# Kernel optimization log

Measured on AMD Instinct MI355X. Metric: run time of the kernel, lower is better.

Reference implementation:

```python
import jax, jax.numpy as jnp
import numpy as np

EPS = 1e-5  # BatchNorm1d default eps
N1, N2 = 4096, 4096


def _encoder(x, W1, b1, W2, b2, W3, b3, gamma, beta):
    # fc1: Linear(node_num,256)+ReLU; fc2: Linear(256,128)+ReLU; fc3: Linear(128,64)+BN(train-mode)+ReLU
    h = jax.nn.relu(x @ W1.T + b1)
    h = jax.nn.relu(h @ W2.T + b2)
    h = h @ W3.T + b3
    m = h.mean(axis=0)
    v = ((h - m) ** 2).mean(axis=0)  # biased variance, as BN training mode
    return jax.nn.relu((h - m) / jnp.sqrt(v + EPS) * gamma + beta)


def _self_attention(x, adj, alpha):
    # vectorized form of the per-node double loop:
    # tmp_i = (sum_{j: adj[i,j]==1} alpha[i,j] * x[j]) / degree_i + x[i]  if degree_i != 0 else 0
    mask = (adj == 1.0).astype(x.dtype)           # [N,N]
    deg = adj.sum(axis=1, keepdims=True)          # [N,1]
    agg = (mask * alpha) @ x                      # [N,64] masked SpMM
    return jnp.where(deg != 0, agg / deg + x, jnp.zeros((), x.dtype))


def setup_inputs() -> dict:
    key = jax.random.key(0)
    ks = jax.random.split(key, 20)
    d = {}
    d["x1"] = jax.random.normal(ks[0], (N1, N1), jnp.float32)
    d["x2"] = jax.random.normal(ks[1], (N2, N2), jnp.float32)
    d["adj1"] = jax.random.bernoulli(ks[2], 0.01, (N1, N1)).astype(jnp.float32)
    d["adj2"] = jax.random.bernoulli(ks[3], 0.01, (N2, N2)).astype(jnp.float32)
    def lin(k, fan_out, fan_in):
        bound = 1.0 / np.sqrt(fan_in)
        k1, k2 = jax.random.split(k)
        return (jax.random.uniform(k1, (fan_out, fan_in), jnp.float32, -bound, bound),
                jax.random.uniform(k2, (fan_out,), jnp.float32, -bound, bound))
    d["e1_W1"], d["e1_b1"] = lin(ks[4], 256, N1)
    d["e1_W2"], d["e1_b2"] = lin(ks[5], 128, 256)
    d["e1_W3"], d["e1_b3"] = lin(ks[6], 64, 128)
    d["e1_gamma"] = jnp.ones((64,), jnp.float32)
    d["e1_beta"] = jnp.zeros((64,), jnp.float32)
    d["e2_W1"], d["e2_b1"] = lin(ks[7], 256, N2)
    d["e2_W2"], d["e2_b2"] = lin(ks[8], 128, 256)
    d["e2_W3"], d["e2_b3"] = lin(ks[9], 64, 128)
    d["e2_gamma"] = jnp.ones((64,), jnp.float32)
    d["e2_beta"] = jnp.zeros((64,), jnp.float32)
    d["alpha1"] = jax.random.uniform(ks[10], (N1, N1), jnp.float32)
    d["alpha2"] = jax.random.uniform(ks[11], (N2, N2), jnp.float32)
    d["Wc"], d["bc"] = lin(ks[12], 2, (N1 + N2) * 64)
    return d


def reference(x1, x2, adj1, adj2,
              e1_W1, e1_b1, e1_W2, e1_b2, e1_W3, e1_b3, e1_gamma, e1_beta,
              e2_W1, e2_b1, e2_W2, e2_b2, e2_W3, e2_b3, e2_gamma, e2_beta,
              alpha1, alpha2, Wc, bc):
    h1 = _encoder(x1, e1_W1, e1_b1, e1_W2, e1_b2, e1_W3, e1_b3, e1_gamma, e1_beta)
    h2 = _encoder(x2, e2_W1, e2_b1, e2_W2, e2_b2, e2_W3, e2_b3, e2_gamma, e2_beta)
    h1 = _self_attention(h1, adj1, alpha1)
    h2 = _self_attention(h2, adj2, alpha2)
    feat = jnp.concatenate([h1, h2], axis=0).reshape(1, -1)  # [1,(N1+N2)*64]
    return feat @ Wc.T + bc  # [1,2] logits (softmax is defined but unused in forward)
```

## Files before the change

### kernel.cpp

```cpp
#include <hip/hip_runtime.h>
#include <cstddef>


#define NN 4096
#define HDIM 64
#define ENC_OUT (NN * HDIM)

typedef _Float16 half8 __attribute__((ext_vector_type(8)));
typedef _Float16 half4 __attribute__((ext_vector_type(4)));
typedef float v4f __attribute__((ext_vector_type(4)));

struct GemmP {
    const void*     A[2];
    const _Float16* B[2];
    const float*    bias[2];
    void*           C[2];
};

template<int NI, bool A_HALF, bool RELU, bool HALF_OUT>
__global__ __launch_bounds__(256) void gemm32_kernel(GemmP p, int K)
{
    constexpr int N = NI * 64;
    __shared__ _Float16 As[32][40];
    __shared__ _Float16 Bs[N][40];

    const int tid = threadIdx.x;
    const int wave = tid >> 6, lane = tid & 63;
    const int quad = lane >> 4, l16 = lane & 15;
    const int enc = blockIdx.z;
    const int m0 = blockIdx.y * 32;

    const _Float16* __restrict__ Bp = p.B[enc];

    const int ar = tid >> 3, ak = (tid & 7) * 4;
    const int br = tid >> 2, bk = (tid & 3) * 8;

    v4f acc[2][NI];
#pragma unroll
    for (int mi = 0; mi < 2; mi++)
#pragma unroll
        for (int ni = 0; ni < NI; ni++) acc[mi][ni] = (v4f){0.f, 0.f, 0.f, 0.f};

    for (int k0 = 0; k0 < K; k0 += 32) {
        __syncthreads();
        if (A_HALF) {
            const _Float16* ap = (const _Float16*)p.A[enc] + (size_t)(m0 + ar) * K + k0 + ak;
            *(half4*)&As[ar][ak] = *(const half4*)ap;
        } else {
            const float* ap = (const float*)p.A[enc] + (size_t)(m0 + ar) * K + k0 + ak;
            float4 a = *(const float4*)ap;
            half4 h;
            h[0] = (_Float16)a.x; h[1] = (_Float16)a.y;
            h[2] = (_Float16)a.z; h[3] = (_Float16)a.w;
            *(half4*)&As[ar][ak] = h;
        }
#pragma unroll
        for (int pass = 0; pass < NI; pass++) {
            const _Float16* bp = Bp + (size_t)(pass * 64 + br) * K + k0 + bk;
            *(half8*)&Bs[pass * 64 + br][bk] = *(const half8*)bp;
        }
        __syncthreads();

        half8 af0 = *(half8*)&As[l16][quad * 8];
        half8 af1 = *(half8*)&As[16 + l16][quad * 8];
#pragma unroll
        for (int ni = 0; ni < NI; ni++) {
            half8 bf = *(half8*)&Bs[wave * NI * 16 + ni * 16 + l16][quad * 8];
            acc[0][ni] = __builtin_amdgcn_mfma_f32_16x16x32_f16(af0, bf, acc[0][ni], 0, 0, 0);
            acc[1][ni] = __builtin_amdgcn_mfma_f32_16x16x32_f16(af1, bf, acc[1][ni], 0, 0, 0);
        }
    }

#pragma unroll
    for (int mi = 0; mi < 2; mi++)
#pragma unroll
        for (int ni = 0; ni < NI; ni++) {
            const int col = wave * NI * 16 + ni * 16 + l16;
            const float bv = p.bias[enc][col];
#pragma unroll
            for (int i = 0; i < 4; i++) {
                const int row = m0 + mi * 16 + quad * 4 + i;
                float v = acc[mi][ni][i] + bv;
                if (RELU) v = fmaxf(v, 0.f);
                if (HALF_OUT)
                    ((_Float16*)p.C[enc])[(size_t)row * N + col] = (_Float16)v;
                else
                    ((float*)p.C[enc])[(size_t)row * N + col] = v;
            }
        }
}

__global__ __launch_bounds__(256) void cvt_kernel(const float* __restrict__ s,
                                                  _Float16* __restrict__ d, int n4)
{
    const int i = blockIdx.x * 256 + threadIdx.x;
    if (i < n4) {
        float4 v = ((const float4*)s)[i];
        half4 h;
        h[0] = (_Float16)v.x; h[1] = (_Float16)v.y;
        h[2] = (_Float16)v.z; h[3] = (_Float16)v.w;
        ((half4*)d)[i] = h;
    }
}

__global__ __launch_bounds__(256) void bn_stat1_kernel(const float* __restrict__ h3,
                                                       float* __restrict__ bnp)
{
    const int enc = blockIdx.y, b = blockIdx.x;
    const int c = threadIdx.x & 63, rg = threadIdx.x >> 6;
    const float* h = h3 + (size_t)enc * ENC_OUT + (size_t)b * 128 * HDIM;
    float s = 0.f, q = 0.f;
    for (int r = rg; r < 128; r += 4) {
        float v = h[(size_t)r * HDIM + c];
        s += v; q += v * v;
    }
    __shared__ float ss[4][64], sq[4][64];
    ss[rg][c] = s; sq[rg][c] = q;
    __syncthreads();
    if (threadIdx.x < 64) {
        float S = ss[0][c] + ss[1][c] + ss[2][c] + ss[3][c];
        float Q = sq[0][c] + sq[1][c] + sq[2][c] + sq[3][c];
        bnp[(size_t)(enc * 32 + b) * 128 + c] = S;
        bnp[(size_t)(enc * 32 + b) * 128 + 64 + c] = Q;
    }
}

__global__ void bn_stat2_kernel(const float* __restrict__ bnp, float* __restrict__ stats)
{
    const int enc = blockIdx.x, c = threadIdx.x;
    float s = 0.f, q = 0.f;
    for (int b = 0; b < 32; b++) {
        s += bnp[(size_t)(enc * 32 + b) * 128 + c];
        q += bnp[(size_t)(enc * 32 + b) * 128 + 64 + c];
    }
    float mean = s * (1.f / NN);
    float var = q * (1.f / NN) - mean * mean;
    stats[enc * 128 + c] = mean;
    stats[enc * 128 + 64 + c] = rsqrtf(var + 1e-5f);
}

__global__ __launch_bounds__(256) void bn_apply_kernel(const float* __restrict__ h3,
                                                       const float* __restrict__ stats,
                                                       const float* __restrict__ g0,
                                                       const float* __restrict__ g1,
                                                       const float* __restrict__ be0,
                                                       const float* __restrict__ be1,
                                                       float* __restrict__ hn)
{
    const int idx = blockIdx.x * 256 + threadIdx.x;
    const int enc = idx >> 18;
    const int c = idx & 63;
    const float* g = enc ? g1 : g0;
    const float* be = enc ? be1 : be0;
    const float m = stats[enc * 128 + c];
    const float rs = stats[enc * 128 + 64 + c];
    float v = (h3[idx] - m) * rs * g[c] + be[c];
    hn[idx] = fmaxf(v, 0.f);
}

__global__ __launch_bounds__(256) void att_kernel(const float* __restrict__ adj1,
                                                  const float* __restrict__ adj2,
                                                  const float* __restrict__ al1,
                                                  const float* __restrict__ al2,
                                                  const float* __restrict__ hn,
                                                  float* __restrict__ out)
{
    const int enc = blockIdx.y;
    const float* adj = enc ? adj2 : adj1;
    const float* al = enc ? al2 : al1;
    const float* h = hn + (size_t)enc * ENC_OUT;
    float* o = out + (size_t)enc * ENC_OUT;
    const int i = blockIdx.x;
    const int tid = threadIdx.x;

    __shared__ int s_cnt;
    __shared__ int s_j[128];
    __shared__ float s_w[128];
    __shared__ float s_acc[4][64];

    if (tid == 0) s_cnt = 0;
    __syncthreads();

    const float* arow = adj + (size_t)i * NN;
    const int jb = tid * 16;
#pragma unroll
    for (int q = 0; q < 4; q++) {
        float4 a = *(const float4*)&arow[jb + q * 4];
        if (a.x == 1.f) { int p = atomicAdd(&s_cnt, 1); if (p < 128) s_j[p] = jb + q * 4 + 0; }
        if (a.y == 1.f) { int p = atomicAdd(&s_cnt, 1); if (p < 128) s_j[p] = jb + q * 4 + 1; }
        if (a.z == 1.f) { int p = atomicAdd(&s_cnt, 1); if (p < 128) s_j[p] = jb + q * 4 + 2; }
        if (a.w == 1.f) { int p = atomicAdd(&s_cnt, 1); if (p < 128) s_j[p] = jb + q * 4 + 3; }
    }
    __syncthreads();
    const int cnt = min(s_cnt, 128);

    const float* alrow = al + (size_t)i * NN;
    for (int t = tid; t < cnt; t += 256) s_w[t] = alrow[s_j[t]];
    __syncthreads();

    const int c = tid & 63;
    const int g = tid >> 6;
    float acc = 0.f;
    for (int t = g; t < cnt; t += 4) acc += s_w[t] * h[(size_t)s_j[t] * HDIM + c];
    s_acc[g][c] = acc;
    __syncthreads();

    if (tid < 64) {
        float r;
        if (cnt != 0) {
            r = (s_acc[0][c] + s_acc[1][c] + s_acc[2][c] + s_acc[3][c]) / (float)cnt
                + h[(size_t)i * HDIM + c];
        } else {
            r = 0.f;
        }
        o[(size_t)i * HDIM + c] = r;
    }
}

#define FDIM (2 * ENC_OUT)

__global__ __launch_bounds__(256) void final_partial_kernel(const float* __restrict__ feat,
                                                            const float* __restrict__ Wc,
                                                            float* __restrict__ partial)
{
    const int gt = blockIdx.x * 256 + threadIdx.x;
    float p0 = 0.f, p1 = 0.f;
    for (int f = gt; f < FDIM; f += 32768) {
        float x = feat[f];
        p0 += x * Wc[f];
        p1 += x * Wc[FDIM + f];
    }
    __shared__ float r0[256], r1[256];
    r0[threadIdx.x] = p0;
    r1[threadIdx.x] = p1;
    __syncthreads();
    for (int off = 128; off > 0; off >>= 1) {
        if (threadIdx.x < off) {
            r0[threadIdx.x] += r0[threadIdx.x + off];
            r1[threadIdx.x] += r1[threadIdx.x + off];
        }
        __syncthreads();
    }
    if (threadIdx.x == 0) {
        partial[blockIdx.x * 2 + 0] = r0[0];
        partial[blockIdx.x * 2 + 1] = r1[0];
    }
}

__global__ void final_reduce_kernel(const float* __restrict__ partial,
                                    const float* __restrict__ bc,
                                    float* __restrict__ out)
{
    const int t = threadIdx.x;
    if (t < 2) {
        float s = bc[t];
        for (int b = 0; b < 128; b++) s += partial[b * 2 + t];
        out[t] = s;
    }
}


extern "C" void kernel_launch(void* const* d_in, const int* in_sizes, int n_in,
                              void* d_out, int out_size, void* d_ws, size_t ws_size,
                              hipStream_t stream)
{
    const float* x1    = (const float*)d_in[0];
    const float* x2    = (const float*)d_in[1];
    const float* adj1  = (const float*)d_in[2];
    const float* adj2  = (const float*)d_in[3];
    const float* e1_W1 = (const float*)d_in[4];
    const float* e1_b1 = (const float*)d_in[5];
    const float* e1_W2 = (const float*)d_in[6];
    const float* e1_b2 = (const float*)d_in[7];
    const float* e1_W3 = (const float*)d_in[8];
    const float* e1_b3 = (const float*)d_in[9];
    const float* e1_g  = (const float*)d_in[10];
    const float* e1_be = (const float*)d_in[11];
    const float* e2_W1 = (const float*)d_in[12];
    const float* e2_b1 = (const float*)d_in[13];
    const float* e2_W2 = (const float*)d_in[14];
    const float* e2_b2 = (const float*)d_in[15];
    const float* e2_W3 = (const float*)d_in[16];
    const float* e2_b3 = (const float*)d_in[17];
    const float* e2_g  = (const float*)d_in[18];
    const float* e2_be = (const float*)d_in[19];
    const float* alpha1 = (const float*)d_in[20];
    const float* alpha2 = (const float*)d_in[21];
    const float* Wc    = (const float*)d_in[22];
    const float* bc    = (const float*)d_in[23];
    (void)in_sizes; (void)n_in; (void)out_size; (void)ws_size;

    char* w = (char*)d_ws;
    _Float16* W1h = (_Float16*)w;  w += (size_t)2 * 256 * NN * 2;
    _Float16* W2h = (_Float16*)w;  w += (size_t)2 * 128 * 256 * 2;
    _Float16* W3h = (_Float16*)w;  w += (size_t)2 * 64 * 128 * 2;
    _Float16* h1h = (_Float16*)w;  w += (size_t)2 * NN * 256 * 2;
    _Float16* h2h = (_Float16*)w;  w += (size_t)2 * NN * 128 * 2;
    float* h3  = (float*)w;        w += (size_t)2 * ENC_OUT * 4;
    float* hn  = (float*)w;        w += (size_t)2 * ENC_OUT * 4;
    float* att = (float*)w;        w += (size_t)2 * ENC_OUT * 4;
    float* bnp = (float*)w;        w += (size_t)2 * 32 * 128 * 4;
    float* stats = (float*)w;      w += 256 * 4;
    float* hpart = (float*)w;      w += 256 * 4;

    const dim3 blk(256);

    cvt_kernel<<<dim3(1024), blk, 0, stream>>>(e1_W1, W1h,               262144);
    cvt_kernel<<<dim3(1024), blk, 0, stream>>>(e2_W1, W1h + 256 * NN,    262144);
    cvt_kernel<<<dim3(32),   blk, 0, stream>>>(e1_W2, W2h,               8192);
    cvt_kernel<<<dim3(32),   blk, 0, stream>>>(e2_W2, W2h + 128 * 256,   8192);
    cvt_kernel<<<dim3(8),    blk, 0, stream>>>(e1_W3, W3h,               2048);
    cvt_kernel<<<dim3(8),    blk, 0, stream>>>(e2_W3, W3h + 64 * 128,    2048);

    GemmP p1 = { {x1, x2}, {W1h, W1h + 256 * NN}, {e1_b1, e2_b1},
                 {h1h, h1h + (size_t)NN * 256} };
    gemm32_kernel<4, false, true, true><<<dim3(1, NN / 32, 2), blk, 0, stream>>>(p1, NN);

    GemmP p2 = { {h1h, h1h + (size_t)NN * 256}, {W2h, W2h + 128 * 256}, {e1_b2, e2_b2},
                 {h2h, h2h + (size_t)NN * 128} };
    gemm32_kernel<2, true, true, true><<<dim3(1, NN / 32, 2), blk, 0, stream>>>(p2, 256);

    GemmP p3 = { {h2h, h2h + (size_t)NN * 128}, {W3h, W3h + 64 * 128}, {e1_b3, e2_b3},
                 {h3, h3 + ENC_OUT} };
    gemm32_kernel<1, true, false, false><<<dim3(1, NN / 32, 2), blk, 0, stream>>>(p3, 128);

    bn_stat1_kernel<<<dim3(32, 2), blk, 0, stream>>>(h3, bnp);
    bn_stat2_kernel<<<dim3(2), dim3(64), 0, stream>>>(bnp, stats);
    bn_apply_kernel<<<dim3(2 * ENC_OUT / 256), blk, 0, stream>>>(h3, stats, e1_g, e2_g,
                                                                 e1_be, e2_be, hn);

    att_kernel<<<dim3(NN, 2), blk, 0, stream>>>(adj1, adj2, alpha1, alpha2, hn, att);

    final_partial_kernel<<<dim3(128), blk, 0, stream>>>(att, Wc, hpart);
    final_reduce_kernel<<<dim3(1), dim3(64), 0, stream>>>(hpart, bc, (float*)d_out);
}
```

Measured before the change: 514.5 us.

## Rework GEMMs with direct global-to-LDS loads, register prefetch, and split-K fc1

The GEMM kernel now loads B tiles straight into LDS with global_load_lds, drops the A shared-memory tile in favour of register-prefetched A fragments, and removes the __syncthreads barriers, relying on per-wave private LDS regions and waitcnt. fc1 is split along K into two halves with fp16 partials, followed by a reduce kernel that adds bias and applies ReLU. The six weight-conversion launches are merged into one, workspace buffers are aliased, and the final dot-product partial kernel uses four times as many blocks. This targets load latency and the low parallelism of the large fc1 GEMM, at the cost of extra partial traffic and fp16 rounding of the partial sums.

```diff
diff --git a/kernel.cpp b/kernel.cpp
--- a/kernel.cpp
+++ b/kernel.cpp
@@ -1,5 +1,6 @@
 #include <hip/hip_runtime.h>
 #include <cstddef>
+#include <cstdint>
 
 
 #define NN 4096
@@ -9,6 +10,12 @@
 typedef _Float16 half8 __attribute__((ext_vector_type(8)));
 typedef _Float16 half4 __attribute__((ext_vector_type(4)));
 typedef float v4f __attribute__((ext_vector_type(4)));
+
+__device__ __forceinline__ void gld_lds16(const void* g, void* l) {
+    __builtin_amdgcn_global_load_lds(
+        (const __attribute__((address_space(1))) void*)g,
+        (__attribute__((address_space(3))) void*)l, 16, 0, 0);
+}
 
 struct GemmP {
     const void*     A[2];
@@ -17,23 +24,41 @@
     void*           C[2];
 };
 
-template<int NI, bool A_HALF, bool RELU, bool HALF_OUT>
-__global__ __launch_bounds__(256) void gemm32_kernel(GemmP p, int K)
+template<int NI, bool A16, int OUT, bool RELU>
+__global__ __launch_bounds__(256) void gemm_kernel(GemmP p, int M, int lda, int Ksub)
 {
     constexpr int N = NI * 64;
-    __shared__ _Float16 As[32][40];
-    __shared__ _Float16 Bs[N][40];
+    __shared__ char Bs[NI * 4 * 1024];
 
     const int tid = threadIdx.x;
     const int wave = tid >> 6, lane = tid & 63;
-    const int quad = lane >> 4, l16 = lane & 15;
-    const int enc = blockIdx.z;
+    const int l16 = lane & 15, quad = lane >> 4;
+    const int enc = blockIdx.z, split = blockIdx.x;
     const int m0 = blockIdx.y * 32;
+    const int kOff = split * Ksub;
+    const int nsteps = Ksub >> 5;
 
     const _Float16* __restrict__ Bp = p.B[enc];
-
-    const int ar = tid >> 3, ak = (tid & 7) * 4;
-    const int br = tid >> 2, bk = (tid & 3) * 8;
+    const char* Abase = (const char*)p.A[enc];
+
+    const size_t aoff0 = (size_t)(m0 + l16) * lda + kOff + quad * 8;
+    const size_t aoff1 = aoff0 + (size_t)16 * lda;
+
+    half8 na0, na1;
+    float4 nf0lo, nf0hi, nf1lo, nf1hi;
+    auto loadA = [&](int s) {
+        if constexpr (A16) {
+            const _Float16* A = (const _Float16*)Abase;
+            na0 = *(const half8*)(A + aoff0 + s * 32);
+            na1 = *(const half8*)(A + aoff1 + s * 32);
+        } else {
+            const float* A = (const float*)Abase;
+            nf0lo = *(const float4*)(A + aoff0 + s * 32);
+            nf0hi = *(const float4*)(A + aoff0 + s * 32 + 4);
+            nf1lo = *(const float4*)(A + aoff1 + s * 32);
+            nf1hi = *(const float4*)(A + aoff1 + s * 32 + 4);
+        }
+    };
 
     v4f acc[2][NI];
 #pragma unroll
@@ -41,33 +66,37 @@
 #pragma unroll
         for (int ni = 0; ni < NI; ni++) acc[mi][ni] = (v4f){0.f, 0.f, 0.f, 0.f};
 
-    for (int k0 = 0; k0 < K; k0 += 32) {
-        __syncthreads();
-        if (A_HALF) {
-            const _Float16* ap = (const _Float16*)p.A[enc] + (size_t)(m0 + ar) * K + k0 + ak;
-            *(half4*)&As[ar][ak] = *(const half4*)ap;
+    loadA(0);
+
+    for (int s = 0; s < nsteps; ++s) {
+#pragma unroll
+        for (int ni = 0; ni < NI; ni++) {
+            const int T = wave * NI + ni;
+            const _Float16* g = Bp + (size_t)(T * 16 + l16) * lda + kOff + s * 32 + quad * 8;
+            gld_lds16(g, &Bs[T * 1024]);
+        }
+        half8 ca0, ca1;
+        if constexpr (A16) {
+            ca0 = na0; ca1 = na1;
         } else {
-            const float* ap = (const float*)p.A[enc] + (size_t)(m0 + ar) * K + k0 + ak;
-            float4 a = *(const float4*)ap;
-            half4 h;
-            h[0] = (_Float16)a.x; h[1] = (_Float16)a.y;
-            h[2] = (_Float16)a.z; h[3] = (_Float16)a.w;
-            *(half4*)&As[ar][ak] = h;
-        }
-#pragma unroll
-        for (int pass = 0; pass < NI; pass++) {
-            const _Float16* bp = Bp + (size_t)(pass * 64 + br) * K + k0 + bk;
-            *(half8*)&Bs[pass * 64 + br][bk] = *(const half8*)bp;
-        }
-        __syncthreads();
-
-        half8 af0 = *(half8*)&As[l16][quad * 8];
-        half8 af1 = *(half8*)&As[16 + l16][quad * 8];
+            ca0[0] = (_Float16)nf0lo.x; ca0[1] = (_Float16)nf0lo.y;
+            ca0[2] = (_Float16)nf0lo.z; ca0[3] = (_Float16)nf0lo.w;
+            ca0[4] = (_Float16)nf0hi.x; ca0[5] = (_Float16)nf0hi.y;
+            ca0[6] = (_Float16)nf0hi.z; ca0[7] = (_Float16)nf0hi.w;
+            ca1[0] = (_Float16)nf1lo.x; ca1[1] = (_Float16)nf1lo.y;
+            ca1[2] = (_Float16)nf1lo.z; ca1[3] = (_Float16)nf1lo.w;
+            ca1[4] = (_Float16)nf1hi.x; ca1[5] = (_Float16)nf1hi.y;
+            ca1[6] = (_Float16)nf1hi.z; ca1[7] = (_Float16)nf1hi.w;
+        }
+        if (s + 1 < nsteps) loadA(s + 1);
+
+        __builtin_amdgcn_s_waitcnt(0x0F70);
+
 #pragma unroll
         for (int ni = 0; ni < NI; ni++) {
-            half8 bf = *(half8*)&Bs[wave * NI * 16 + ni * 16 + l16][quad * 8];
-            acc[0][ni] = __builtin_amdgcn_mfma_f32_16x16x32_f16(af0, bf, acc[0][ni], 0, 0, 0);
-            acc[1][ni] = __builtin_amdgcn_mfma_f32_16x16x32_f16(af1, bf, acc[1][ni], 0, 0, 0);
+            half8 bf = *(const half8*)&Bs[(wave * NI + ni) * 1024 + lane * 16];
+            acc[0][ni] = __builtin_amdgcn_mfma_f32_16x16x32_f16(ca0, bf, acc[0][ni], 0, 0, 0);
+            acc[1][ni] = __builtin_amdgcn_mfma_f32_16x16x32_f16(ca1, bf, acc[1][ni], 0, 0, 0);
         }
     }
 
@@ -76,30 +105,66 @@
 #pragma unroll
         for (int ni = 0; ni < NI; ni++) {
             const int col = wave * NI * 16 + ni * 16 + l16;
-            const float bv = p.bias[enc][col];
 #pragma unroll
             for (int i = 0; i < 4; i++) {
                 const int row = m0 + mi * 16 + quad * 4 + i;
-                float v = acc[mi][ni][i] + bv;
-                if (RELU) v = fmaxf(v, 0.f);
-                if (HALF_OUT)
-                    ((_Float16*)p.C[enc])[(size_t)row * N + col] = (_Float16)v;
-                else
-                    ((float*)p.C[enc])[(size_t)row * N + col] = v;
+                float v = acc[mi][ni][i];
+                if constexpr (OUT == 2) {
+                    ((_Float16*)p.C[0])[((size_t)(split * 2 + enc) * M + row) * N + col]
+                        = (_Float16)v;
+                } else {
+                    v += p.bias[enc][col];
+                    if (RELU) v = fmaxf(v, 0.f);
+                    if constexpr (OUT == 0)
+                        ((_Float16*)p.C[enc])[(size_t)row * N + col] = (_Float16)v;
+                    else
+                        ((float*)p.C[enc])[(size_t)row * N + col] = v;
+                }
             }
         }
 }
 
-__global__ __launch_bounds__(256) void cvt_kernel(const float* __restrict__ s,
-                                                  _Float16* __restrict__ d, int n4)
-{
-    const int i = blockIdx.x * 256 + threadIdx.x;
-    if (i < n4) {
-        float4 v = ((const float4*)s)[i];
-        half4 h;
-        h[0] = (_Float16)v.x; h[1] = (_Float16)v.y;
-        h[2] = (_Float16)v.z; h[3] = (_Float16)v.w;
-        ((half4*)d)[i] = h;
+__global__ __launch_bounds__(256) void fc1_reduce_kernel(const _Float16* __restrict__ part,
+                                                         const float* __restrict__ b0,
+                                                         const float* __restrict__ b1,
+                                                         _Float16* __restrict__ h1h)
+{
+    const size_t i = ((size_t)blockIdx.x * 256 + threadIdx.x) * 8;
+    const int e = (int)(i >> 20);
+    const size_t r = i & ((1u << 20) - 1);
+    half8 p0 = *(const half8*)&part[((size_t)(0 * 2 + e) << 20) + r];
+    half8 p1 = *(const half8*)&part[((size_t)(1 * 2 + e) << 20) + r];
+    const int col = (int)(i & 255);
+    const float* bs = e ? b1 : b0;
+    float4 ba = *(const float4*)&bs[col];
+    float4 bb = *(const float4*)&bs[col + 4];
+    float b[8] = {ba.x, ba.y, ba.z, ba.w, bb.x, bb.y, bb.z, bb.w};
+    half8 o;
+#pragma unroll
+    for (int j = 0; j < 8; j++) {
+        float v = (float)p0[j] + (float)p1[j] + b[j];
+        o[j] = (_Float16)fmaxf(v, 0.f);
+    }
+    *(half8*)&h1h[i] = o;
+}
+
+struct CvtJob { const float* s; _Float16* d; int n4; };
+struct CvtP { CvtJob j[6]; };
+
+__global__ __launch_bounds__(256) void cvt_all_kernel(CvtP p)
+{
+    int i = blockIdx.x * 256 + threadIdx.x;
+#pragma unroll
+    for (int k = 0; k < 6; k++) {
+        if (i < p.j[k].n4) {
+            float4 v = ((const float4*)p.j[k].s)[i];
+            half4 h;
+            h[0] = (_Float16)v.x; h[1] = (_Float16)v.y;
+            h[2] = (_Float16)v.z; h[3] = (_Float16)v.w;
+            ((half4*)p.j[k].d)[i] = h;
+            return;
+        }
+        i -= p.j[k].n4;
     }
 }
 
@@ -225,7 +290,7 @@
 {
     const int gt = blockIdx.x * 256 + threadIdx.x;
     float p0 = 0.f, p1 = 0.f;
-    for (int f = gt; f < FDIM; f += 32768) {
+    for (int f = gt; f < FDIM; f += 131072) {
         float x = feat[f];
         p0 += x * Wc[f];
         p1 += x * Wc[FDIM + f];
@@ -254,7 +319,7 @@
     const int t = threadIdx.x;
     if (t < 2) {
         float s = bc[t];
-        for (int b = 0; b < 128; b++) s += partial[b * 2 + t];
+        for (int b = 0; b < 512; b++) s += partial[b * 2 + t];
         out[t] = s;
     }
 }
@@ -295,34 +360,39 @@
     _Float16* W2h = (_Float16*)w;  w += (size_t)2 * 128 * 256 * 2;
     _Float16* W3h = (_Float16*)w;  w += (size_t)2 * 64 * 128 * 2;
     _Float16* h1h = (_Float16*)w;  w += (size_t)2 * NN * 256 * 2;
-    _Float16* h2h = (_Float16*)w;  w += (size_t)2 * NN * 128 * 2;
-    float* h3  = (float*)w;        w += (size_t)2 * ENC_OUT * 4;
-    float* hn  = (float*)w;        w += (size_t)2 * ENC_OUT * 4;
-    float* att = (float*)w;        w += (size_t)2 * ENC_OUT * 4;
+    char* shared8 = w;             w += (size_t)8 * 1024 * 1024;
     float* bnp = (float*)w;        w += (size_t)2 * 32 * 128 * 4;
     float* stats = (float*)w;      w += 256 * 4;
-    float* hpart = (float*)w;      w += 256 * 4;
+    float* hpart = (float*)w;      w += 1024 * 4;
+
+    _Float16* part = (_Float16*)shared8;
+    _Float16* h2h  = (_Float16*)shared8;
+    float* h3  = (float*)(shared8 + 2 * 1024 * 1024);
+    float* hn  = (float*)(shared8 + 4 * 1024 * 1024);
+    float* att = (float*)(shared8 + 6 * 1024 * 1024);
 
     const dim3 blk(256);
 
-    cvt_kernel<<<dim3(1024), blk, 0, stream>>>(e1_W1, W1h,               262144);
-    cvt_kernel<<<dim3(1024), blk, 0, stream>>>(e2_W1, W1h + 256 * NN,    262144);
-    cvt_kernel<<<dim3(32),   blk, 0, stream>>>(e1_W2, W2h,               8192);
-    cvt_kernel<<<dim3(32),   blk, 0, stream>>>(e2_W2, W2h + 128 * 256,   8192);
-    cvt_kernel<<<dim3(8),    blk, 0, stream>>>(e1_W3, W3h,               2048);
-    cvt_kernel<<<dim3(8),    blk, 0, stream>>>(e2_W3, W3h + 64 * 128,    2048);
-
-    GemmP p1 = { {x1, x2}, {W1h, W1h + 256 * NN}, {e1_b1, e2_b1},
-                 {h1h, h1h + (size_t)NN * 256} };
-    gemm32_kernel<4, false, true, true><<<dim3(1, NN / 32, 2), blk, 0, stream>>>(p1, NN);
+    CvtP cp;
+    cp.j[0] = { e1_W1, W1h,             262144 };
+    cp.j[1] = { e2_W1, W1h + 256 * NN,  262144 };
+    cp.j[2] = { e1_W2, W2h,             8192 };
+    cp.j[3] = { e2_W2, W2h + 128 * 256, 8192 };
+    cp.j[4] = { e1_W3, W3h,             2048 };
+    cp.j[5] = { e2_W3, W3h + 64 * 128,  2048 };
+    cvt_all_kernel<<<dim3(2128), blk, 0, stream>>>(cp);
+
+    GemmP p1 = { {x1, x2}, {W1h, W1h + 256 * NN}, {e1_b1, e2_b1}, {part, part} };
+    gemm_kernel<4, false, 2, false><<<dim3(2, NN / 32, 2), blk, 0, stream>>>(p1, NN, NN, 2048);
+    fc1_reduce_kernel<<<dim3(1024), blk, 0, stream>>>(part, e1_b1, e2_b1, h1h);
 
     GemmP p2 = { {h1h, h1h + (size_t)NN * 256}, {W2h, W2h + 128 * 256}, {e1_b2, e2_b2},
                  {h2h, h2h + (size_t)NN * 128} };
-    gemm32_kernel<2, true, true, true><<<dim3(1, NN / 32, 2), blk, 0, stream>>>(p2, 256);
+    gemm_kernel<2, true, 0, true><<<dim3(1, NN / 32, 2), blk, 0, stream>>>(p2, NN, 256, 256);
 
     GemmP p3 = { {h2h, h2h + (size_t)NN * 128}, {W3h, W3h + 64 * 128}, {e1_b3, e2_b3},
                  {h3, h3 + ENC_OUT} };
-    gemm32_kernel<1, true, false, false><<<dim3(1, NN / 32, 2), blk, 0, stream>>>(p3, 128);
+    gemm_kernel<1, true, 1, false><<<dim3(1, NN / 32, 2), blk, 0, stream>>>(p3, NN, 128, 128);
 
     bn_stat1_kernel<<<dim3(32, 2), blk, 0, stream>>>(h3, bnp);
     bn_stat2_kernel<<<dim3(2), dim3(64), 0, stream>>>(bnp, stats);
@@ -331,6 +401,6 @@
 
     att_kernel<<<dim3(NN, 2), blk, 0, stream>>>(adj1, adj2, alpha1, alpha2, hn, att);
 
-    final_partial_kernel<<<dim3(128), blk, 0, stream>>>(att, Wc, hpart);
+    final_partial_kernel<<<dim3(512), blk, 0, stream>>>(att, Wc, hpart);
     final_reduce_kernel<<<dim3(1), dim3(64), 0, stream>>>(hpart, bc, (float*)d_out);
 }
```

Result: no change. 514.5 us (-0.0%).

## Split-K register GEMM, fuse BN apply into attention, merge weight conversions

Applied to the files above, without the earlier changes.

The GEMM is rewritten with 1024-thread blocks that split K across four wave groups. Operands load straight from global memory into registers with one step of prefetch, and the partial sums are reduced through shared memory, which removes the per-step LDS staging and barriers. The six weight-conversion launches become one kernel. The BatchNorm apply pass is folded into the attention kernel, which now does one row per wave and finds neighbours by ballot over the adjacency row, dropping the shared-memory atomics and the 128-neighbour cap. The final reduction is spread over more blocks. The costs are higher register pressure and uncoalesced per-lane global loads in the GEMM, plus a serial per-neighbour loop in attention.

```diff
diff --git a/kernel.cpp b/kernel.cpp
--- a/kernel.cpp
+++ b/kernel.cpp
@@ -1,5 +1,6 @@
 #include <hip/hip_runtime.h>
 #include <cstddef>
+#include <cstdint>
 
 
 #define NN 4096
@@ -17,23 +18,49 @@
     void*           C[2];
 };
 
-template<int NI, bool A_HALF, bool RELU, bool HALF_OUT>
-__global__ __launch_bounds__(256) void gemm32_kernel(GemmP p, int K)
+template<int NI, bool A16, bool HALF_OUT, bool RELU>
+__global__ __launch_bounds__(1024) void gemm_kernel(GemmP p, int K)
 {
     constexpr int N = NI * 64;
-    __shared__ _Float16 As[32][40];
-    __shared__ _Float16 Bs[N][40];
-
-    const int tid = threadIdx.x;
+    __shared__ float red[8 * NI * 512];
+
+    const int tid  = threadIdx.x;
     const int wave = tid >> 6, lane = tid & 63;
-    const int quad = lane >> 4, l16 = lane & 15;
-    const int enc = blockIdx.z;
-    const int m0 = blockIdx.y * 32;
+    const int l16  = lane & 15, quad = lane >> 4;
+    const int cg   = wave & 3;
+    const int kg   = wave >> 2;
+    const int enc  = blockIdx.y;
+    const int m0   = blockIdx.x * 32;
+
+    const int Kq    = K >> 2;
+    const int steps = Kq >> 5;
+    const int kbase = kg * Kq + quad * 8;
 
     const _Float16* __restrict__ Bp = p.B[enc];
 
-    const int ar = tid >> 3, ak = (tid & 7) * 4;
-    const int br = tid >> 2, bk = (tid & 3) * 8;
+    half8  nb[NI];
+    half8  na[2];
+    float4 nf[4];
+
+    auto issue = [&](int s) {
+        const int k = kbase + s * 32;
+#pragma unroll
+        for (int ni = 0; ni < NI; ni++) {
+            const int col = cg * (NI * 16) + ni * 16 + l16;
+            nb[ni] = *(const half8*)(Bp + (size_t)col * K + k);
+        }
+        if constexpr (A16) {
+            const _Float16* A = (const _Float16*)p.A[enc];
+            na[0] = *(const half8*)(A + (size_t)(m0 + l16) * K + k);
+            na[1] = *(const half8*)(A + (size_t)(m0 + 16 + l16) * K + k);
+        } else {
+            const float* A = (const float*)p.A[enc];
+            nf[0] = *(const float4*)(A + (size_t)(m0 + l16) * K + k);
+            nf[1] = *(const float4*)(A + (size_t)(m0 + l16) * K + k + 4);
+            nf[2] = *(const float4*)(A + (size_t)(m0 + 16 + l16) * K + k);
+            nf[3] = *(const float4*)(A + (size_t)(m0 + 16 + l16) * K + k + 4);
+        }
+    };
 
     v4f acc[2][NI];
 #pragma unroll
@@ -41,65 +68,102 @@
 #pragma unroll
         for (int ni = 0; ni < NI; ni++) acc[mi][ni] = (v4f){0.f, 0.f, 0.f, 0.f};
 
-    for (int k0 = 0; k0 < K; k0 += 32) {
-        __syncthreads();
-        if (A_HALF) {
-            const _Float16* ap = (const _Float16*)p.A[enc] + (size_t)(m0 + ar) * K + k0 + ak;
-            *(half4*)&As[ar][ak] = *(const half4*)ap;
+    issue(0);
+
+    for (int s = 0; s < steps; s++) {
+        half8 a0, a1;
+        if constexpr (A16) {
+            a0 = na[0]; a1 = na[1];
         } else {
-            const float* ap = (const float*)p.A[enc] + (size_t)(m0 + ar) * K + k0 + ak;
-            float4 a = *(const float4*)ap;
+            a0[0] = (_Float16)nf[0].x; a0[1] = (_Float16)nf[0].y;
+            a0[2] = (_Float16)nf[0].z; a0[3] = (_Float16)nf[0].w;
+            a0[4] = (_Float16)nf[1].x; a0[5] = (_Float16)nf[1].y;
+            a0[6] = (_Float16)nf[1].z; a0[7] = (_Float16)nf[1].w;
+            a1[0] = (_Float16)nf[2].x; a1[1] = (_Float16)nf[2].y;
+            a1[2] = (_Float16)nf[2].z; a1[3] = (_Float16)nf[2].w;
+            a1[4] = (_Float16)nf[3].x; a1[5] = (_Float16)nf[3].y;
+            a1[6] = (_Float16)nf[3].z; a1[7] = (_Float16)nf[3].w;
+        }
+        half8 cb[NI];
+#pragma unroll
+        for (int ni = 0; ni < NI; ni++) cb[ni] = nb[ni];
+
+        if (s + 1 < steps) issue(s + 1);
+
+#pragma unroll
+        for (int ni = 0; ni < NI; ni++) {
+            acc[0][ni] = __builtin_amdgcn_mfma_f32_16x16x32_f16(a0, cb[ni], acc[0][ni], 0, 0, 0);
+            acc[1][ni] = __builtin_amdgcn_mfma_f32_16x16x32_f16(a1, cb[ni], acc[1][ni], 0, 0, 0);
+        }
+    }
+
+    auto dump = [&](int region) {
+#pragma unroll
+        for (int mi = 0; mi < 2; mi++)
+#pragma unroll
+            for (int ni = 0; ni < NI; ni++)
+#pragma unroll
+                for (int i = 0; i < 4; i++)
+                    red[region * (512 * NI) + ((mi * NI + ni) * 4 + i) * 64 + lane]
+                        = acc[mi][ni][i];
+    };
+    auto gather = [&](int region) {
+#pragma unroll
+        for (int mi = 0; mi < 2; mi++)
+#pragma unroll
+            for (int ni = 0; ni < NI; ni++)
+#pragma unroll
+                for (int i = 0; i < 4; i++)
+                    acc[mi][ni][i]
+                        += red[region * (512 * NI) + ((mi * NI + ni) * 4 + i) * 64 + lane];
+    };
+
+    if (kg >= 2) dump((kg - 2) * 4 + cg);
+    __syncthreads();
+    if (kg < 2) gather(kg * 4 + cg);
+    __syncthreads();
+    if (kg == 1) dump(cg);
+    __syncthreads();
+
+    if (kg == 0) {
+        gather(cg);
+#pragma unroll
+        for (int mi = 0; mi < 2; mi++)
+#pragma unroll
+            for (int ni = 0; ni < NI; ni++) {
+                const int col = cg * (NI * 16) + ni * 16 + l16;
+                const float bv = p.bias[enc][col];
+#pragma unroll
+                for (int i = 0; i < 4; i++) {
+                    const int row = m0 + mi * 16 + quad * 4 + i;
+                    float v = acc[mi][ni][i] + bv;
+                    if (RELU) v = fmaxf(v, 0.f);
+                    if constexpr (HALF_OUT)
+                        ((_Float16*)p.C[enc])[(size_t)row * N + col] = (_Float16)v;
+                    else
+                        ((float*)p.C[enc])[(size_t)row * N + col] = v;
+                }
+            }
+    }
+}
+
+struct CvtJob { const float* s; _Float16* d; int n4; };
+struct CvtP { CvtJob j[6]; };
+
+__global__ __launch_bounds__(256) void cvt_all_kernel(CvtP p)
+{
+    int i = blockIdx.x * 256 + threadIdx.x;
+#pragma unroll
+    for (int k = 0; k < 6; k++) {
+        if (i < p.j[k].n4) {
+            float4 v = ((const float4*)p.j[k].s)[i];
             half4 h;
-            h[0] = (_Float16)a.x; h[1] = (_Float16)a.y;
-            h[2] = (_Float16)a.z; h[3] = (_Float16)a.w;
-            *(half4*)&As[ar][ak] = h;
-        }
-#pragma unroll
-        for (int pass = 0; pass < NI; pass++) {
-            const _Float16* bp = Bp + (size_t)(pass * 64 + br) * K + k0 + bk;
-            *(half8*)&Bs[pass * 64 + br][bk] = *(const half8*)bp;
-        }
-        __syncthreads();
-
-        half8 af0 = *(half8*)&As[l16][quad * 8];
-        half8 af1 = *(half8*)&As[16 + l16][quad * 8];
-#pragma unroll
-        for (int ni = 0; ni < NI; ni++) {
-            half8 bf = *(half8*)&Bs[wave * NI * 16 + ni * 16 + l16][quad * 8];
-            acc[0][ni] = __builtin_amdgcn_mfma_f32_16x16x32_f16(af0, bf, acc[0][ni], 0, 0, 0);
-            acc[1][ni] = __builtin_amdgcn_mfma_f32_16x16x32_f16(af1, bf, acc[1][ni], 0, 0, 0);
-        }
-    }
-
-#pragma unroll
-    for (int mi = 0; mi < 2; mi++)
-#pragma unroll
-        for (int ni = 0; ni < NI; ni++) {
-            const int col = wave * NI * 16 + ni * 16 + l16;
-            const float bv = p.bias[enc][col];
-#pragma unroll
-            for (int i = 0; i < 4; i++) {
-                const int row = m0 + mi * 16 + quad * 4 + i;
-                float v = acc[mi][ni][i] + bv;
-                if (RELU) v = fmaxf(v, 0.f);
-                if (HALF_OUT)
-                    ((_Float16*)p.C[enc])[(size_t)row * N + col] = (_Float16)v;
-                else
-                    ((float*)p.C[enc])[(size_t)row * N + col] = v;
-            }
-        }
-}
-
-__global__ __launch_bounds__(256) void cvt_kernel(const float* __restrict__ s,
-                                                  _Float16* __restrict__ d, int n4)
-{
-    const int i = blockIdx.x * 256 + threadIdx.x;
-    if (i < n4) {
-        float4 v = ((const float4*)s)[i];
-        half4 h;
-        h[0] = (_Float16)v.x; h[1] = (_Float16)v.y;
-        h[2] = (_Float16)v.z; h[3] = (_Float16)v.w;
-        ((half4*)d)[i] = h;
+            h[0] = (_Float16)v.x; h[1] = (_Float16)v.y;
+            h[2] = (_Float16)v.z; h[3] = (_Float16)v.w;
+            ((half4*)p.j[k].d)[i] = h;
+            return;
+        }
+        i -= p.j[k].n4;
     }
 }
 
@@ -139,82 +203,53 @@
     stats[enc * 128 + 64 + c] = rsqrtf(var + 1e-5f);
 }
 
-__global__ __launch_bounds__(256) void bn_apply_kernel(const float* __restrict__ h3,
-                                                       const float* __restrict__ stats,
-                                                       const float* __restrict__ g0,
-                                                       const float* __restrict__ g1,
-                                                       const float* __restrict__ be0,
-                                                       const float* __restrict__ be1,
-                                                       float* __restrict__ hn)
-{
-    const int idx = blockIdx.x * 256 + threadIdx.x;
-    const int enc = idx >> 18;
-    const int c = idx & 63;
-    const float* g = enc ? g1 : g0;
-    const float* be = enc ? be1 : be0;
-    const float m = stats[enc * 128 + c];
-    const float rs = stats[enc * 128 + 64 + c];
-    float v = (h3[idx] - m) * rs * g[c] + be[c];
-    hn[idx] = fmaxf(v, 0.f);
-}
-
 __global__ __launch_bounds__(256) void att_kernel(const float* __restrict__ adj1,
                                                   const float* __restrict__ adj2,
                                                   const float* __restrict__ al1,
                                                   const float* __restrict__ al2,
-                                                  const float* __restrict__ hn,
+                                                  const float* __restrict__ h3,
+                                                  const float* __restrict__ stats,
+                                                  const float* __restrict__ g0,
+                                                  const float* __restrict__ g1,
+                                                  const float* __restrict__ be0,
+                                                  const float* __restrict__ be1,
                                                   float* __restrict__ out)
 {
     const int enc = blockIdx.y;
+    const int i = blockIdx.x * 4 + (threadIdx.x >> 6);
+    const int c = threadIdx.x & 63;
+
     const float* adj = enc ? adj2 : adj1;
-    const float* al = enc ? al2 : al1;
-    const float* h = hn + (size_t)enc * ENC_OUT;
-    float* o = out + (size_t)enc * ENC_OUT;
-    const int i = blockIdx.x;
-    const int tid = threadIdx.x;
-
-    __shared__ int s_cnt;
-    __shared__ int s_j[128];
-    __shared__ float s_w[128];
-    __shared__ float s_acc[4][64];
-
-    if (tid == 0) s_cnt = 0;
-    __syncthreads();
+    const float* al  = enc ? al2 : al1;
+    const float* h   = h3 + (size_t)enc * ENC_OUT;
+
+    const float m  = stats[enc * 128 + c];
+    const float rs = stats[enc * 128 + 64 + c];
+    const float ga = (enc ? g1 : g0)[c];
+    const float bb = (enc ? be1 : be0)[c];
+    const float sa = rs * ga;
+    const float sb = bb - m * sa;
 
     const float* arow = adj + (size_t)i * NN;
-    const int jb = tid * 16;
-#pragma unroll
-    for (int q = 0; q < 4; q++) {
-        float4 a = *(const float4*)&arow[jb + q * 4];
-        if (a.x == 1.f) { int p = atomicAdd(&s_cnt, 1); if (p < 128) s_j[p] = jb + q * 4 + 0; }
-        if (a.y == 1.f) { int p = atomicAdd(&s_cnt, 1); if (p < 128) s_j[p] = jb + q * 4 + 1; }
-        if (a.z == 1.f) { int p = atomicAdd(&s_cnt, 1); if (p < 128) s_j[p] = jb + q * 4 + 2; }
-        if (a.w == 1.f) { int p = atomicAdd(&s_cnt, 1); if (p < 128) s_j[p] = jb + q * 4 + 3; }
-    }
-    __syncthreads();
-    const int cnt = min(s_cnt, 128);
-
-    const float* alrow = al + (size_t)i * NN;
-    for (int t = tid; t < cnt; t += 256) s_w[t] = alrow[s_j[t]];
-    __syncthreads();
-
-    const int c = tid & 63;
-    const int g = tid >> 6;
+    const float* wrow = al + (size_t)i * NN;
+
     float acc = 0.f;
-    for (int t = g; t < cnt; t += 4) acc += s_w[t] * h[(size_t)s_j[t] * HDIM + c];
-    s_acc[g][c] = acc;
-    __syncthreads();
-
-    if (tid < 64) {
-        float r;
-        if (cnt != 0) {
-            r = (s_acc[0][c] + s_acc[1][c] + s_acc[2][c] + s_acc[3][c]) / (float)cnt
-                + h[(size_t)i * HDIM + c];
-        } else {
-            r = 0.f;
-        }
-        o[(size_t)i * HDIM + c] = r;
-    }
+    int cnt = 0;
+    for (int base = 0; base < NN; base += 64) {
+        const float a = arow[base + c];
+        unsigned long long mask = __ballot(a == 1.0f);
+        cnt += __popcll(mask);
+        while (mask) {
+            const int j = base + (int)__builtin_ctzll(mask);
+            mask &= mask - 1;
+            const float wj = wrow[j];
+            const float hv = fmaxf(h[(size_t)j * HDIM + c] * sa + sb, 0.f);
+            acc += wj * hv;
+        }
+    }
+    const float hi = fmaxf(h[(size_t)i * HDIM + c] * sa + sb, 0.f);
+    out[(size_t)enc * ENC_OUT + (size_t)i * HDIM + c]
+        = cnt ? acc / (float)cnt + hi : 0.f;
 }
 
 #define FDIM (2 * ENC_OUT)
@@ -225,7 +260,7 @@
 {
     const int gt = blockIdx.x * 256 + threadIdx.x;
     float p0 = 0.f, p1 = 0.f;
-    for (int f = gt; f < FDIM; f += 32768) {
+    for (int f = gt; f < FDIM; f += 131072) {
         float x = feat[f];
         p0 += x * Wc[f];
         p1 += x * Wc[FDIM + f];
@@ -254,7 +289,7 @@
     const int t = threadIdx.x;
     if (t < 2) {
         float s = bc[t];
-        for (int b = 0; b < 128; b++) s += partial[b * 2 + t];
+        for (int b = 0; b < 512; b++) s += partial[b * 2 + t];
         out[t] = s;
     }
 }
@@ -297,40 +332,42 @@
     _Float16* h1h = (_Float16*)w;  w += (size_t)2 * NN * 256 * 2;
     _Float16* h2h = (_Float16*)w;  w += (size_t)2 * NN * 128 * 2;
     float* h3  = (float*)w;        w += (size_t)2 * ENC_OUT * 4;
-    float* hn  = (float*)w;        w += (size_t)2 * ENC_OUT * 4;
     float* att = (float*)w;        w += (size_t)2 * ENC_OUT * 4;
     float* bnp = (float*)w;        w += (size_t)2 * 32 * 128 * 4;
     float* stats = (float*)w;      w += 256 * 4;
-    float* hpart = (float*)w;      w += 256 * 4;
+    float* hpart = (float*)w;      w += 1024 * 4;
 
     const dim3 blk(256);
-
-    cvt_kernel<<<dim3(1024), blk, 0, stream>>>(e1_W1, W1h,               262144);
-    cvt_kernel<<<dim3(1024), blk, 0, stream>>>(e2_W1, W1h + 256 * NN,    262144);
-    cvt_kernel<<<dim3(32),   blk, 0, stream>>>(e1_W2, W2h,               8192);
-    cvt_kernel<<<dim3(32),   blk, 0, stream>>>(e2_W2, W2h + 128 * 256,   8192);
-    cvt_kernel<<<dim3(8),    blk, 0, stream>>>(e1_W3, W3h,               2048);
-    cvt_kernel<<<dim3(8),    blk, 0, stream>>>(e2_W3, W3h + 64 * 128,    2048);
+    const dim3 blk1k(1024);
+
+    CvtP cp;
+    cp.j[0] = { e1_W1, W1h,             262144 };
+    cp.j[1] = { e2_W1, W1h + 256 * NN,  262144 };
+    cp.j[2] = { e1_W2, W2h,             8192 };
+    cp.j[3] = { e2_W2, W2h + 128 * 256, 8192 };
+    cp.j[4] = { e1_W3, W3h,             2048 };
+    cp.j[5] = { e2_W3, W3h + 64 * 128,  2048 };
+    cvt_all_kernel<<<dim3(2128), blk, 0, stream>>>(cp);
 
     GemmP p1 = { {x1, x2}, {W1h, W1h + 256 * NN}, {e1_b1, e2_b1},
                  {h1h, h1h + (size_t)NN * 256} };
-    gemm32_kernel<4, false, true, true><<<dim3(1, NN / 32, 2), blk, 0, stream>>>(p1, NN);
+    gemm_kernel<4, false, true, true><<<dim3(NN / 32, 2), blk1k, 0, stream>>>(p1, NN);
 
     GemmP p2 = { {h1h, h1h + (size_t)NN * 256}, {W2h, W2h + 128 * 256}, {e1_b2, e2_b2},
                  {h2h, h2h + (size_t)NN * 128} };
-    gemm32_kernel<2, true, true, true><<<dim3(1, NN / 32, 2), blk, 0, stream>>>(p2, 256);
+    gemm_kernel<2, true, true, true><<<dim3(NN / 32, 2), blk1k, 0, stream>>>(p2, 256);
 
     GemmP p3 = { {h2h, h2h + (size_t)NN * 128}, {W3h, W3h + 64 * 128}, {e1_b3, e2_b3},
                  {h3, h3 + ENC_OUT} };
-    gemm32_kernel<1, true, false, false><<<dim3(1, NN / 32, 2), blk, 0, stream>>>(p3, 128);
+    gemm_kernel<1, true, false, false><<<dim3(NN / 32, 2), blk1k, 0, stream>>>(p3, 128);
 
     bn_stat1_kernel<<<dim3(32, 2), blk, 0, stream>>>(h3, bnp);
     bn_stat2_kernel<<<dim3(2), dim3(64), 0, stream>>>(bnp, stats);
-    bn_apply_kernel<<<dim3(2 * ENC_OUT / 256), blk, 0, stream>>>(h3, stats, e1_g, e2_g,
-                                                                 e1_be, e2_be, hn);
-
-    att_kernel<<<dim3(NN, 2), blk, 0, stream>>>(adj1, adj2, alpha1, alpha2, hn, att);
-
-    final_partial_kernel<<<dim3(128), blk, 0, stream>>>(att, Wc, hpart);
+
+    att_kernel<<<dim3(NN / 4, 2), blk, 0, stream>>>(adj1, adj2, alpha1, alpha2,
+                                                    h3, stats, e1_g, e2_g, e1_be, e2_be,
+                                                    att);
+
+    final_partial_kernel<<<dim3(512), blk, 0, stream>>>(att, Wc, hpart);
     final_reduce_kernel<<<dim3(1), dim3(64), 0, stream>>>(hpart, bc, (float*)d_out);
 }
```

Result: no change. 521.5 us (+1.4%).
